# Kernel optimization log

Measured on AMD Instinct MI355X. Metric: run time of the kernel, lower is better.

Reference implementation:

```python
import jax, jax.numpy as jnp
import numpy as np

B, S, DIM = 4, 2048, 512
HEADS, DHEAD = 8, 64
INNER = HEADS * DHEAD


def setup_inputs() -> dict:
    key = jax.random.key(0)
    k1, k2, k3, k4 = jax.random.split(key, 4)
    x = jax.random.normal(k1, (B, S, DIM), dtype=jnp.float32)
    W_qkv = jax.random.normal(k2, (DIM, 3 * INNER), dtype=jnp.float32) * (DIM ** -0.5)
    W_out = jax.random.normal(k3, (INNER, DIM), dtype=jnp.float32) * (INNER ** -0.5)
    b_out = jnp.zeros((DIM,), dtype=jnp.float32)
    # learnable log-temperature, initialized to log(dim_head**-0.5)
    log_temp = jnp.asarray(np.log(DHEAD ** -0.5), dtype=jnp.float32)
    return {"x": x, "W_qkv": W_qkv, "log_temp": log_temp, "W_out": W_out, "b_out": b_out}


def reference(x, W_qkv, log_temp, W_out, b_out):
    b, s, _ = x.shape
    qkv = x @ W_qkv  # [b, s, 3*inner]
    q, k, v = jnp.split(qkv, 3, axis=-1)
    # [b, s, inner] -> [b, h, s, d]
    reshape = lambda t: t.reshape(b, s, HEADS, DHEAD).transpose(0, 2, 1, 3)
    q, k, v = reshape(q), reshape(k), reshape(v)
    dots = jnp.einsum("bhid,bhjd->bhij", q, k) * jnp.exp(log_temp)
    mask_value = -jnp.finfo(dots.dtype).max
    eye = jnp.eye(s, dtype=bool)
    dots = jnp.where(eye, mask_value, dots)
    attn = jax.nn.softmax(dots, axis=-1)
    out = jnp.einsum("bhij,bhjd->bhid", attn, v)
    out = out.transpose(0, 2, 1, 3).reshape(b, s, INNER)
    return out @ W_out + b_out
```

## Files before the change

kernel.cpp:

```cpp
#include <hip/hip_runtime.h>
#include <hip/hip_bf16.h>

#define BB 4
#define SS 2048
#define DIMM 512
#define HH 8
#define DD 64
#define NQKV 1536

typedef float  floatx4 __attribute__((ext_vector_type(4)));
typedef short  bf16x8  __attribute__((ext_vector_type(8)));
typedef short  bf16x4  __attribute__((ext_vector_type(4)));

#define MFMA16(A, B, C) __builtin_amdgcn_mfma_f32_16x16x32_bf16(A, B, C, 0, 0, 0)

__device__ __forceinline__ unsigned short f2bf(float f) {
    unsigned int u = __float_as_uint(f);
    u += 0x7FFFu + ((u >> 16) & 1u);
    return (unsigned short)(u >> 16);
}

__device__ __forceinline__ unsigned int f2bf_pk(float lo, float hi) {
    float2 f; f.x = lo; f.y = hi;
    __hip_bfloat162 h = __float22bfloat162_rn(f);
    return *reinterpret_cast<unsigned int*>(&h);
}

__device__ __forceinline__ float fast_exp2(float x) {
#if __has_builtin(__builtin_amdgcn_exp2f)
    return __builtin_amdgcn_exp2f(x);
#else
    return __exp2f(x);
#endif
}

__device__ __forceinline__ void gl_lds16(const void* g, void* l) {
    __builtin_amdgcn_global_load_lds(
        (__attribute__((address_space(1))) void*)g,
        (__attribute__((address_space(3))) void*)l,
        16, 0, 0);
}

__global__ __launch_bounds__(256) void k_prep(
    const float* __restrict__ x, const float* __restrict__ W_qkv,
    const float* __restrict__ W_out,
    unsigned short* __restrict__ xb, unsigned short* __restrict__ Wq_t,
    unsigned short* __restrict__ Wo_t) {
    __shared__ float t[32][33];
    int bid = blockIdx.x, tid = threadIdx.x;
    if (bid < 4096) {
        int i = (bid * 256 + tid) * 4;
        float4 v = *(const float4*)(x + i);
        ushort4 o;
        o.x = f2bf(v.x); o.y = f2bf(v.y); o.z = f2bf(v.z); o.w = f2bf(v.w);
        *(ushort4*)(xb + i) = o;
        return;
    }
    const float* in; unsigned short* out; int R = 512, C, bx, by;
    if (bid < 4864) { in = W_qkv; out = Wq_t; C = 1536; int blk = bid - 4096; bx = blk % 48; by = blk / 48; }
    else            { in = W_out; out = Wo_t; C = 512;  int blk = bid - 4864; bx = blk % 16; by = blk / 16; }
    int tx = tid & 31, ty = tid >> 5;
    int c0 = bx * 32, r0 = by * 32;
    for (int i = 0; i < 4; i++) {
        int r = r0 + ty + i * 8;
        t[ty + i * 8][tx] = in[(size_t)r * C + c0 + tx];
    }
    __syncthreads();
    for (int i = 0; i < 4; i++) {
        int cc = c0 + ty + i * 8;
        out[(size_t)cc * R + r0 + tx] = f2bf(t[tx][ty + i * 8]);
    }
}

__global__ __launch_bounds__(256) void k_gemm_qkv(
    const unsigned short* __restrict__ A,
    const unsigned short* __restrict__ Bt,
    const float* __restrict__ log_temp,
    unsigned short* __restrict__ Qb,
    unsigned short* __restrict__ Kb,
    unsigned short* __restrict__ Vt) {
    __shared__ unsigned short smem[2][128 * 64];
    unsigned short* As = smem[0];
    unsigned short* Bs = smem[1];
    const int K = 512;
    int bid = blockIdx.x;
    int swz = (bid & 7) * 96 + (bid >> 3);
    int local = swz % 96;
    int m_blk = (swz / 96) * 8 + (local & 7);
    int n_blk = local >> 3;
    int m0 = m_blk * 128, n0 = n_blk * 128;
    int tid = threadIdx.x;
    int w = tid >> 6, lane = tid & 63;
    int c = lane & 15, q4 = lane >> 4;
    int wm = w >> 1, wn = w & 1;
    float qscale = __expf(log_temp[0]) * 1.44269504f;

    floatx4 acc[4][4] = {};

    for (int k0 = 0; k0 < K; k0 += 64) {
        __syncthreads();
        for (int i = 0; i < 4; i++) {
            int cidx = w * 256 + i * 64 + lane;
            int row = cidx >> 3, cc = cidx & 7;
            int gcc = cc ^ (row & 7);
            gl_lds16(A + (size_t)(m0 + row) * K + k0 + gcc * 8,
                     As + (size_t)(w * 256 + i * 64) * 8);
            gl_lds16(Bt + (size_t)(n0 + row) * K + k0 + gcc * 8,
                     Bs + (size_t)(w * 256 + i * 64) * 8);
        }
        __syncthreads();
        bf16x8 aF[2][4], bF[2][4];
        for (int kh = 0; kh < 2; kh++)
            for (int mt = 0; mt < 4; mt++) {
                int row = wm * 64 + mt * 16 + c;
                aF[kh][mt] = *(const bf16x8*)&As[row * 64 + (((kh * 4 + q4) ^ (row & 7)) * 8)];
            }
        for (int kh = 0; kh < 2; kh++)
            for (int nt = 0; nt < 4; nt++) {
                int row = wn * 64 + nt * 16 + c;
                bF[kh][nt] = *(const bf16x8*)&Bs[row * 64 + (((kh * 4 + q4) ^ (row & 7)) * 8)];
            }
        for (int kh = 0; kh < 2; kh++)
            for (int mt = 0; mt < 4; mt++)
                for (int nt = 0; nt < 4; nt++)
                    acc[mt][nt] = MFMA16(aF[kh][mt], bF[kh][nt], acc[mt][nt]);
    }

    if (n0 < 1024) {
        for (int nt = 0; nt < 4; nt++) {
            int n = n0 + wn * 64 + nt * 16 + c;
            int t = n >> 9, inner = n & 511;
            int h = inner >> 6, d = inner & 63;
            for (int mt = 0; mt < 4; mt++) {
                for (int r = 0; r < 4; r++) {
                    int m = m0 + wm * 64 + mt * 16 + q4 * 4 + r;
                    int b = m >> 11, s = m & 2047;
                    int bh = b * 8 + h;
                    float v = acc[mt][nt][r];
                    if (t == 0)  Qb[((size_t)bh * SS + s) * 64 + d] = f2bf(v * qscale);
                    else         Kb[((size_t)bh * SS + s) * 64 + d] = f2bf(v);
                }
            }
        }
    } else {
        unsigned short* T = &smem[0][0];
        int b = m0 >> 11, s_base = m0 & 2047;
        for (int half = 0; half < 2; half++) {
            __syncthreads();
            if (wn == half) {
                for (int nt = 0; nt < 4; nt++)
                    for (int mt = 0; mt < 4; mt++)
                        for (int r = 0; r < 4; r++)
                            T[(nt * 16 + c) * 136 + wm * 64 + mt * 16 + q4 * 4 + r] =
                                f2bf(acc[mt][nt][r]);
            }
            __syncthreads();
            for (int rr = 0; rr < 4; rr++) {
                int nl = w * 16 + rr * 4 + q4;
                int ml = c * 8;
                bf16x8 v = *(const bf16x8*)&T[nl * 136 + ml];
                int n = n0 + half * 64 + nl;
                int h = (n >> 6) - 16, d = n & 63;
                int bh = b * 8 + h;
                *(bf16x8*)(Vt + ((size_t)bh * 64 + d) * SS + s_base + ml) = v;
            }
        }
    }
}

__global__ __launch_bounds__(512, 4) void k_attn(
    const unsigned short* __restrict__ Qb,
    const unsigned short* __restrict__ Kb,
    const unsigned short* __restrict__ Vt,
    unsigned short* __restrict__ AO) {
    __shared__ unsigned short KVs[2][2][2][64 * 64];
    int bid = blockIdx.x;
    int swz = (bid & 7) * 64 + (bid >> 3);
    int q0 = (swz & 15) * 128;
    int bh = swz >> 4;
    int h = bh & 7, b = bh >> 3;
    int tid = threadIdx.x, w = tid >> 6, lane = tid & 63;
    int wg = w >> 2, wi = w & 3;
    int c = lane & 15, q4 = lane >> 4;

    const unsigned short* Kbase = Kb + (size_t)bh * SS * 64 + (size_t)wg * 1024 * 64;
    const unsigned short* Vbase = Vt + (size_t)bh * 64 * SS;

    bf16x8 qf[2][2];
    for (int mt = 0; mt < 2; mt++) {
        const unsigned short* qp = Qb + ((size_t)bh * SS + q0 + wi * 32 + mt * 16 + c) * 64;
        qf[mt][0] = *(const bf16x8*)(qp + q4 * 8);
        qf[mt][1] = *(const bf16x8*)(qp + 32 + q4 * 8);
    }
    bf16x8 ones;
    for (int i = 0; i < 8; i++) ones[i] = (short)0x3F80;

    int cidx0 = wi * 128 + lane, cidx1 = cidx0 + 64;
    int row0 = cidx0 >> 3, cc0 = cidx0 & 7;
    int row1 = cidx1 >> 3, cc1 = cidx1 & 7;
    int fk0 = (row0 & 3) | ((row0 >> 1) & 4);
    int fk1 = (row1 & 3) | ((row1 >> 1) & 4);
    const unsigned short* ksrc0 = Kbase + (size_t)row0 * 64 + (cc0 ^ fk0) * 8;
    const unsigned short* ksrc1 = Kbase + (size_t)row1 * 64 + (cc1 ^ fk1) * 8;
    const unsigned short* vsrc0 = Vbase + (size_t)row0 * SS + wg * 1024 + (cc0 ^ (row0 & 7)) * 8;
    const unsigned short* vsrc1 = Vbase + (size_t)row1 * SS + wg * 1024 + (cc1 ^ (row1 & 7)) * 8;
    unsigned short* kdst0 = &KVs[0][wg][0][0] + wi * 1024;
    unsigned short* kdst1 = kdst0 + 512;
    unsigned short* vdst0 = &KVs[1][wg][0][0] + wi * 1024;
    unsigned short* vdst1 = vdst0 + 512;

    gl_lds16(ksrc0, kdst0); gl_lds16(ksrc1, kdst1);
    gl_lds16(vsrc0, vdst0); gl_lds16(vsrc1, vdst1);

    int mask_j0 = (q0 + wi * 32) & ~63;
    int mglob0 = q0 + wi * 32 + c;
    int mglob1 = mglob0 + 16;
    floatx4 oacc[2][4] = {};
    floatx4 osum[2] = {};

    for (int jt = 0; jt < 16; jt++) {
        int buf = jt & 1;
        int j0 = wg * 1024 + jt * 64;
        __syncthreads();
        if (jt + 1 < 16) {
            int jl = (jt + 1) * 64;
            gl_lds16(ksrc0 + (size_t)jl * 64, kdst0 + (buf ^ 1) * 4096);
            gl_lds16(ksrc1 + (size_t)jl * 64, kdst1 + (buf ^ 1) * 4096);
            gl_lds16(vsrc0 + jl, vdst0 + (buf ^ 1) * 4096);
            gl_lds16(vsrc1 + jl, vdst1 + (buf ^ 1) * 4096);
        }
        bool diag = (j0 == mask_j0);
        const unsigned short* Ksb = &KVs[0][wg][buf][0];
        const unsigned short* Vsb = &KVs[1][wg][buf][0];

        for (int g = 0; g < 2; g++) {
            bf16x8 kf[2][2];
            for (int inner = 0; inner < 2; inner++) {
                int row = g * 32 + ((c >> 2) << 3) + inner * 4 + (c & 3);
                kf[inner][0] = *(const bf16x8*)&Ksb[row * 64 + ((q4 ^ (c & 7)) * 8)];
                kf[inner][1] = *(const bf16x8*)&Ksb[row * 64 + (((4 + q4) ^ (c & 7)) * 8)];
            }
            bf16x8 vf[4];
            for (int dt = 0; dt < 4; dt++) {
                int vrow = dt * 16 + c;
                vf[dt] = *(const bf16x8*)&Vsb[vrow * 64 + (((g * 4 + q4) ^ (c & 7)) * 8)];
            }

            floatx4 sa[2][2];
            __builtin_amdgcn_s_setprio(1);
            for (int mt = 0; mt < 2; mt++)
                for (int inner = 0; inner < 2; inner++) {
                    floatx4 t = {};
                    t = MFMA16(kf[inner][0], qf[mt][0], t);
                    t = MFMA16(kf[inner][1], qf[mt][1], t);
                    sa[mt][inner] = t;
                }
            __builtin_amdgcn_s_setprio(0);

            if (diag) {
                for (int inner = 0; inner < 2; inner++)
                    for (int r = 0; r < 4; r++) {
                        int jg = j0 + g * 32 + q4 * 8 + inner * 4 + r;
                        if (jg == mglob0) sa[0][inner][r] = -1e30f;
                        if (jg == mglob1) sa[1][inner][r] = -1e30f;
                    }
            }

            for (int mt = 0; mt < 2; mt++) {
                float e0 = fast_exp2(sa[mt][0][0]), e1 = fast_exp2(sa[mt][0][1]);
                float e2 = fast_exp2(sa[mt][0][2]), e3 = fast_exp2(sa[mt][0][3]);
                float e4 = fast_exp2(sa[mt][1][0]), e5 = fast_exp2(sa[mt][1][1]);
                float e6 = fast_exp2(sa[mt][1][2]), e7 = fast_exp2(sa[mt][1][3]);
                union { bf16x8 v; unsigned int u[4]; } P;
                P.u[0] = f2bf_pk(e0, e1); P.u[1] = f2bf_pk(e2, e3);
                P.u[2] = f2bf_pk(e4, e5); P.u[3] = f2bf_pk(e6, e7);
                __builtin_amdgcn_s_setprio(1);
                for (int dt = 0; dt < 4; dt++)
                    oacc[mt][dt] = MFMA16(P.v, vf[dt], oacc[mt][dt]);
                osum[mt] = MFMA16(P.v, ones, osum[mt]);
                __builtin_amdgcn_s_setprio(0);
            }
        }
    }

    __syncthreads();
    float* p = (float*)&KVs[0][0][0][0] + ((size_t)(wi * 64 + lane)) * 41;
    if (wg == 1) {
        for (int mt = 0; mt < 2; mt++)
            for (int dt = 0; dt < 4; dt++)
                for (int r = 0; r < 4; r++)
                    p[mt * 16 + dt * 4 + r] = oacc[mt][dt][r];
        for (int mt = 0; mt < 2; mt++)
            for (int r = 0; r < 4; r++)
                p[32 + mt * 4 + r] = osum[mt][r];
    }
    __syncthreads();
    if (wg == 0) {
        for (int mt = 0; mt < 2; mt++)
            for (int dt = 0; dt < 4; dt++)
                for (int r = 0; r < 4; r++)
                    oacc[mt][dt][r] += p[mt * 16 + dt * 4 + r];
        for (int mt = 0; mt < 2; mt++)
            for (int r = 0; r < 4; r++)
                osum[mt][r] += p[32 + mt * 4 + r];

        for (int mt = 0; mt < 2; mt++) {
            for (int r = 0; r < 4; r++) {
                float inv = 1.0f / osum[mt][r];
                int s = q0 + wi * 32 + mt * 16 + q4 * 4 + r;
                for (int dt = 0; dt < 4; dt++)
                    AO[((size_t)b * SS + s) * 512 + h * 64 + dt * 16 + c] =
                        f2bf(oacc[mt][dt][r] * inv);
            }
        }
    }
}

__global__ __launch_bounds__(256) void k_gemm_out(
    const unsigned short* __restrict__ A,
    const unsigned short* __restrict__ Bt,
    const float* __restrict__ bias,
    float* __restrict__ out) {
    __shared__ unsigned short As[64 * 64];
    __shared__ unsigned short Bs[128 * 64];
    const int K = 512;
    int m0 = blockIdx.x * 64, n0 = blockIdx.y * 128;
    int tid = threadIdx.x;
    int w = tid >> 6, lane = tid & 63;
    int c = lane & 15, q4 = lane >> 4;

    floatx4 acc[8] = {};

    for (int k0 = 0; k0 < K; k0 += 64) {
        __syncthreads();
        for (int i = 0; i < 2; i++) {
            int cidx = i * 256 + tid;
            int row = cidx >> 3, cc = cidx & 7;
            int gcc = cc ^ (row & 7);
            gl_lds16(A + (size_t)(m0 + row) * K + k0 + gcc * 8,
                     As + (size_t)(i * 256 + w * 64) * 8);
        }
        for (int i = 0; i < 4; i++) {
            int cidx = i * 256 + tid;
            int row = cidx >> 3, cc = cidx & 7;
            int gcc = cc ^ (row & 7);
            gl_lds16(Bt + (size_t)(n0 + row) * K + k0 + gcc * 8,
                     Bs + (size_t)(i * 256 + w * 64) * 8);
        }
        __syncthreads();
        bf16x8 aF[2], bF[2][8];
        for (int kh = 0; kh < 2; kh++) {
            int row = w * 16 + c;
            aF[kh] = *(const bf16x8*)&As[row * 64 + (((kh * 4 + q4) ^ (row & 7)) * 8)];
        }
        for (int kh = 0; kh < 2; kh++)
            for (int nt = 0; nt < 8; nt++) {
                int row = nt * 16 + c;
                bF[kh][nt] = *(const bf16x8*)&Bs[row * 64 + (((kh * 4 + q4) ^ (row & 7)) * 8)];
            }
        for (int kh = 0; kh < 2; kh++)
            for (int nt = 0; nt < 8; nt++)
                acc[nt] = MFMA16(aF[kh], bF[kh][nt], acc[nt]);
    }

    for (int nt = 0; nt < 8; nt++) {
        int n = n0 + nt * 16 + c;
        float bv = bias[n];
        for (int r = 0; r < 4; r++) {
            int m = m0 + w * 16 + q4 * 4 + r;
            out[(size_t)m * 512 + n] = acc[nt][r] + bv;
        }
    }
}

extern "C" void kernel_launch(void* const* d_in, const int* in_sizes, int n_in,
                              void* d_out, int out_size, void* d_ws, size_t ws_size,
                              hipStream_t stream) {
    const float* x        = (const float*)d_in[0];
    const float* W_qkv    = (const float*)d_in[1];
    const float* log_temp = (const float*)d_in[2];
    const float* W_out    = (const float*)d_in[3];
    const float* b_out    = (const float*)d_in[4];
    float* out = (float*)d_out;

    char* ws = (char*)d_ws;
    unsigned short* xb   = (unsigned short*)(ws + 0);
    unsigned short* Wq_t = (unsigned short*)(ws + 8388608);
    unsigned short* Wo_t = (unsigned short*)(ws + 9961472);
    unsigned short* Qb   = (unsigned short*)(ws + 10485760);
    unsigned short* Kb   = (unsigned short*)(ws + 18874368);
    unsigned short* Vt   = (unsigned short*)(ws + 27262976);
    unsigned short* AO   = (unsigned short*)(ws + 35651584);

    k_prep<<<5120, 256, 0, stream>>>(x, W_qkv, W_out, xb, Wq_t, Wo_t);
    k_gemm_qkv<<<768, 256, 0, stream>>>(xb, Wq_t, log_temp, Qb, Kb, Vt);
    k_attn<<<512, 512, 0, stream>>>(Qb, Kb, Vt, AO);
    k_gemm_out<<<dim3(128, 4), 256, 0, stream>>>(AO, Wo_t, b_out, out);
}
```

Measured before the change: 149.5 us.

## Batch QK MFMAs per tile, use native bf16 pack, drop QKV GEMM swizzle

In the attention loop, all QK^T MFMAs for both 32-key groups are now issued before any exp/PV work, and the diagonal mask is applied once per tile. The goal is longer independent MFMA runs so that exp and conversion latency can overlap them. The float-to-bf16 pack now uses the v_cvt_pk_bf16_f32 instruction through inline asm instead of the HIP intrinsic. The QKV GEMM drops its block-index swizzle in favour of a plain 2D grid, which may hurt L2 reuse, and the attention change raises register pressure.

```diff
diff --git a/kernel.cpp b/kernel.cpp
--- a/kernel.cpp
+++ b/kernel.cpp
@@ -20,10 +20,10 @@
     return (unsigned short)(u >> 16);
 }
 
-__device__ __forceinline__ unsigned int f2bf_pk(float lo, float hi) {
-    float2 f; f.x = lo; f.y = hi;
-    __hip_bfloat162 h = __float22bfloat162_rn(f);
-    return *reinterpret_cast<unsigned int*>(&h);
+__device__ __forceinline__ unsigned int cvtpk(float lo, float hi) {
+    unsigned int r;
+    asm("v_cvt_pk_bf16_f32 %0, %1, %2" : "=v"(r) : "v"(lo), "v"(hi));
+    return r;
 }
 
 __device__ __forceinline__ float fast_exp2(float x) {
@@ -83,12 +83,7 @@
     unsigned short* As = smem[0];
     unsigned short* Bs = smem[1];
     const int K = 512;
-    int bid = blockIdx.x;
-    int swz = (bid & 7) * 96 + (bid >> 3);
-    int local = swz % 96;
-    int m_blk = (swz / 96) * 8 + (local & 7);
-    int n_blk = local >> 3;
-    int m0 = m_blk * 128, n0 = n_blk * 128;
+    int m0 = blockIdx.x * 128, n0 = blockIdx.y * 128;
     int tid = threadIdx.x;
     int w = tid >> 6, lane = tid & 63;
     int c = lane & 15, q4 = lane >> 4;
@@ -194,6 +189,7 @@
     }
     bf16x8 ones;
     for (int i = 0; i < 8; i++) ones[i] = (short)0x3F80;
+    const floatx4 fzero = {};
 
     int cidx0 = wi * 128 + lane, cidx1 = cidx0 + 64;
     int row0 = cidx0 >> 3, cc0 = cidx0 & 7;
@@ -229,10 +225,10 @@
             gl_lds16(vsrc0 + jl, vdst0 + (buf ^ 1) * 4096);
             gl_lds16(vsrc1 + jl, vdst1 + (buf ^ 1) * 4096);
         }
-        bool diag = (j0 == mask_j0);
         const unsigned short* Ksb = &KVs[0][wg][buf][0];
         const unsigned short* Vsb = &KVs[1][wg][buf][0];
 
+        floatx4 sa[2][2][2];
         for (int g = 0; g < 2; g++) {
             bf16x8 kf[2][2];
             for (int inner = 0; inner < 2; inner++) {
@@ -240,40 +236,40 @@
                 kf[inner][0] = *(const bf16x8*)&Ksb[row * 64 + ((q4 ^ (c & 7)) * 8)];
                 kf[inner][1] = *(const bf16x8*)&Ksb[row * 64 + (((4 + q4) ^ (c & 7)) * 8)];
             }
+            __builtin_amdgcn_s_setprio(1);
+            for (int mt = 0; mt < 2; mt++)
+                for (int inner = 0; inner < 2; inner++) {
+                    floatx4 t = MFMA16(kf[inner][0], qf[mt][0], fzero);
+                    t = MFMA16(kf[inner][1], qf[mt][1], t);
+                    sa[g][mt][inner] = t;
+                }
+            __builtin_amdgcn_s_setprio(0);
+        }
+
+        if (j0 == mask_j0) {
+            for (int g = 0; g < 2; g++)
+                for (int inner = 0; inner < 2; inner++)
+                    for (int r = 0; r < 4; r++) {
+                        int jg = j0 + g * 32 + q4 * 8 + inner * 4 + r;
+                        if (jg == mglob0) sa[g][0][inner][r] = -1e30f;
+                        if (jg == mglob1) sa[g][1][inner][r] = -1e30f;
+                    }
+        }
+
+        for (int g = 0; g < 2; g++) {
             bf16x8 vf[4];
             for (int dt = 0; dt < 4; dt++) {
                 int vrow = dt * 16 + c;
                 vf[dt] = *(const bf16x8*)&Vsb[vrow * 64 + (((g * 4 + q4) ^ (c & 7)) * 8)];
             }
-
-            floatx4 sa[2][2];
-            __builtin_amdgcn_s_setprio(1);
-            for (int mt = 0; mt < 2; mt++)
-                for (int inner = 0; inner < 2; inner++) {
-                    floatx4 t = {};
-                    t = MFMA16(kf[inner][0], qf[mt][0], t);
-                    t = MFMA16(kf[inner][1], qf[mt][1], t);
-                    sa[mt][inner] = t;
-                }
-            __builtin_amdgcn_s_setprio(0);
-
-            if (diag) {
-                for (int inner = 0; inner < 2; inner++)
-                    for (int r = 0; r < 4; r++) {
-                        int jg = j0 + g * 32 + q4 * 8 + inner * 4 + r;
-                        if (jg == mglob0) sa[0][inner][r] = -1e30f;
-                        if (jg == mglob1) sa[1][inner][r] = -1e30f;
-                    }
-            }
-
             for (int mt = 0; mt < 2; mt++) {
-                float e0 = fast_exp2(sa[mt][0][0]), e1 = fast_exp2(sa[mt][0][1]);
-                float e2 = fast_exp2(sa[mt][0][2]), e3 = fast_exp2(sa[mt][0][3]);
-                float e4 = fast_exp2(sa[mt][1][0]), e5 = fast_exp2(sa[mt][1][1]);
-                float e6 = fast_exp2(sa[mt][1][2]), e7 = fast_exp2(sa[mt][1][3]);
+                float e0 = fast_exp2(sa[g][mt][0][0]), e1 = fast_exp2(sa[g][mt][0][1]);
+                float e2 = fast_exp2(sa[g][mt][0][2]), e3 = fast_exp2(sa[g][mt][0][3]);
+                float e4 = fast_exp2(sa[g][mt][1][0]), e5 = fast_exp2(sa[g][mt][1][1]);
+                float e6 = fast_exp2(sa[g][mt][1][2]), e7 = fast_exp2(sa[g][mt][1][3]);
                 union { bf16x8 v; unsigned int u[4]; } P;
-                P.u[0] = f2bf_pk(e0, e1); P.u[1] = f2bf_pk(e2, e3);
-                P.u[2] = f2bf_pk(e4, e5); P.u[3] = f2bf_pk(e6, e7);
+                P.u[0] = cvtpk(e0, e1); P.u[1] = cvtpk(e2, e3);
+                P.u[2] = cvtpk(e4, e5); P.u[3] = cvtpk(e6, e7);
                 __builtin_amdgcn_s_setprio(1);
                 for (int dt = 0; dt < 4; dt++)
                     oacc[mt][dt] = MFMA16(P.v, vf[dt], oacc[mt][dt]);
@@ -393,7 +389,7 @@
     unsigned short* AO   = (unsigned short*)(ws + 35651584);
 
     k_prep<<<5120, 256, 0, stream>>>(x, W_qkv, W_out, xb, Wq_t, Wo_t);
-    k_gemm_qkv<<<768, 256, 0, stream>>>(xb, Wq_t, log_temp, Qb, Kb, Vt);
+    k_gemm_qkv<<<dim3(64, 12), 256, 0, stream>>>(xb, Wq_t, log_temp, Qb, Kb, Vt);
     k_attn<<<512, 512, 0, stream>>>(Qb, Kb, Vt, AO);
     k_gemm_out<<<dim3(128, 4), 256, 0, stream>>>(AO, Wo_t, b_out, out);
 }
```

After: 143.3 us. 4.2% less time.
